# Kernel optimization log

Measured on AMD Instinct MI355X. Metric: run time of the kernel, lower is better.

## Reference

```python
import jax, jax.numpy as jnp
import numpy as np

N_NODES = 50000
N_EDGES = 800000
OBS_DIM = 25
HID = 128
EMB = 64
EDGE_DIM = 8
HEADS = 4
N_LAYERS = 3
COMM_RANGE = 1500.0
LN_EPS = 1e-5


def layernorm(x, g, b):
    mu = jnp.mean(x, axis=-1, keepdims=True)
    var = jnp.mean((x - mu) ** 2, axis=-1, keepdims=True)
    return (x - mu) / jnp.sqrt(var + LN_EPS) * g + b


def setup_inputs() -> dict:
    key = jax.random.key(0)
    ks = iter(jax.random.split(key, 64))

    def w(shape, s=0.05):
        return (jax.random.normal(next(ks), shape, jnp.float32) * s).astype(jnp.float32)

    inp = {}
    inp["observations"] = jax.random.normal(next(ks), (N_NODES, OBS_DIM), jnp.float32)
    inp["positions"] = jax.random.uniform(next(ks), (N_NODES, 2), jnp.float32) * 1000.0
    inp["edge_index"] = jax.random.randint(next(ks), (2, N_EDGES), 0, N_NODES, jnp.int32)
    # node encoder (obs_encoder branch: Linear-LN-ReLU-Linear-ReLU)
    inp["enc_w1"] = w((OBS_DIM, HID)); inp["enc_b1"] = w((HID,), 0.01)
    inp["enc_ln_g"] = jnp.ones((HID,), jnp.float32); inp["enc_ln_b"] = jnp.zeros((HID,), jnp.float32)
    inp["enc_w2"] = w((HID, EMB)); inp["enc_b2"] = w((EMB,), 0.01)
    cat_dim = 2 * EMB + EDGE_DIM  # 136
    # per-layer GNN params, stacked over layers
    inp["msg_w1"] = w((N_LAYERS, cat_dim, HID)); inp["msg_b1"] = w((N_LAYERS, HID), 0.01)
    inp["msg_w2"] = w((N_LAYERS, HID, EMB)); inp["msg_b2"] = w((N_LAYERS, EMB), 0.01)
    inp["att_w1"] = w((N_LAYERS, cat_dim, HID)); inp["att_b1"] = w((N_LAYERS, HID), 0.01)
    inp["att_w2"] = w((N_LAYERS, HID, HEADS)); inp["att_b2"] = w((N_LAYERS, HEADS), 0.01)
    inp["upd_w1"] = w((N_LAYERS, 2 * EMB, HID)); inp["upd_b1"] = w((N_LAYERS, HID), 0.01)
    inp["upd_w2"] = w((N_LAYERS, HID, EMB)); inp["upd_b2"] = w((N_LAYERS, EMB), 0.01)
    inp["ln_g"] = jnp.ones((N_LAYERS, EMB), jnp.float32); inp["ln_b"] = jnp.zeros((N_LAYERS, EMB), jnp.float32)
    # output projection
    inp["out_w1"] = w((EMB, HID)); inp["out_b1"] = w((HID,), 0.01)
    inp["out_w2"] = w((HID, EMB)); inp["out_b2"] = w((EMB,), 0.01)
    return inp


def reference(observations, positions, edge_index,
              enc_w1, enc_b1, enc_ln_g, enc_ln_b, enc_w2, enc_b2,
              msg_w1, msg_b1, msg_w2, msg_b2,
              att_w1, att_b1, att_w2, att_b2,
              upd_w1, upd_b1, upd_w2, upd_b2,
              ln_g, ln_b,
              out_w1, out_b1, out_w2, out_b2):
    n = observations.shape[0]
    # --- node encoder (use_full_obs=True path) ---
    h = observations @ enc_w1 + enc_b1
    h = jax.nn.relu(layernorm(h, enc_ln_g, enc_ln_b))
    x = jax.nn.relu(h @ enc_w2 + enc_b2)  # [N, EMB]

    # --- edge features (build_graph math, edges given) ---
    src, dst = edge_index[0], edge_index[1]
    rel = positions[dst] - positions[src]                    # [E, 2]
    dist = jnp.linalg.norm(rel, axis=-1, keepdims=True)      # [E, 1]
    rel_n = rel / (dist + 1e-6)
    dist_n = dist / COMM_RANGE
    angle = jnp.arctan2(rel[:, 1], rel[:, 0])[:, None]
    edge_attr = jnp.concatenate(
        [dist_n, rel_n, jnp.cos(angle), jnp.sin(angle), dist_n ** 2,
         jnp.zeros((rel.shape[0], 2), x.dtype)], axis=-1)    # [E, 8]

    # --- GNN communication layers (PyG: x_i = target = dst, x_j = source = src,
    #     aggregate to dst; dropout inactive at inference) ---
    for l in range(N_LAYERS):
        cat = jnp.concatenate([x[dst], x[src], edge_attr], axis=-1)       # [E, 136]
        m = jax.nn.relu(cat @ msg_w1[l] + msg_b1[l]) @ msg_w2[l] + msg_b2[l]   # [E, EMB]
        a = jax.nn.relu(cat @ att_w1[l] + att_b1[l]) @ att_w2[l] + att_b2[l]   # [E, HEADS]
        wgt = jnp.mean(jax.nn.softmax(a, axis=-1), axis=-1, keepdims=True)     # [E, 1]
        aggr = jax.ops.segment_sum(m * wgt, dst, num_segments=n)               # [N, EMB]
        upd_in = jnp.concatenate([x, aggr], axis=-1)                            # [N, 2*EMB]
        upd = jax.nn.relu(upd_in @ upd_w1[l] + upd_b1[l]) @ upd_w2[l] + upd_b2[l]
        x = layernorm(x + upd, ln_g[l], ln_b[l])

    # --- output projection ---
    return jax.nn.relu(x @ out_w1 + out_b1) @ out_w2 + out_b2
```

## Files before the change

kernel.cpp:

```cpp
#include <hip/hip_runtime.h>
#include <hip/hip_bf16.h>

typedef unsigned short ushort_t;
typedef unsigned int uint_t;

constexpr int OBS  = 25;
constexpr int HID  = 128;
constexpr int EMB  = 64;
constexpr int CAT  = 136;
constexpr int NN   = 50000;
constexpr int HALF = NN / 2;
constexpr int NK   = 2 * NN;

constexpr int TE      = 128;
constexpr int ETHR    = 256;
constexpr int K1PAD   = 148;
constexpr int K2PAD   = 140;
constexpr int K1STEPS = 9;
constexpr int K2STEPS = 8;

constexpr int TB = 128;

typedef __attribute__((ext_vector_type(8)))  short bf16x8;
typedef __attribute__((ext_vector_type(16))) float f32x16;
typedef __attribute__((ext_vector_type(4)))  uint_t uint4v;
typedef __attribute__((ext_vector_type(4)))  float f32x4;

__device__ __forceinline__ ushort_t f2bf(float f) {
    union { float f; uint_t u; } v; v.f = f;
    uint_t r = v.u + 0x7FFFu + ((v.u >> 16) & 1u);
    return (ushort_t)(r >> 16);
}

__device__ __forceinline__ bf16x8 ld8(const ushort_t* p) {
    uint2 lo = *reinterpret_cast<const uint2*>(p);
    uint2 hi = *reinterpret_cast<const uint2*>(p + 4);
    uint4 u = make_uint4(lo.x, lo.y, hi.x, hi.y);
    return __builtin_bit_cast(bf16x8, u);
}

#define CROW(R, LHI) (4 * (LHI) + ((R) & 3) + 8 * ((R) >> 2))

__global__ __launch_bounds__(256) void k_hist(
    const int* __restrict__ src, const int* __restrict__ dst,
    int* __restrict__ hist, int ne)
{
    int e = blockIdx.x * 256 + threadIdx.x;
    if (e < ne) {
        int key = (src[e] >= HALF ? NN : 0) + dst[e];
        atomicAdd(&hist[key], 1);
    }
}

__global__ __launch_bounds__(512) void k_scan1(
    const int* __restrict__ hist, int* __restrict__ scanned,
    int* __restrict__ bsum, int nk)
{
    __shared__ int s[512];
    int t = threadIdx.x, i = blockIdx.x * 512 + t;
    int v = (i < nk) ? hist[i] : 0;
    s[t] = v; __syncthreads();
#pragma unroll
    for (int off = 1; off < 512; off <<= 1) {
        int x = (t >= off) ? s[t - off] : 0;
        __syncthreads();
        s[t] += x;
        __syncthreads();
    }
    if (i < nk) scanned[i] = s[t] - v;
    if (t == 511) bsum[blockIdx.x] = s[511];
}

__global__ __launch_bounds__(512) void k_scan3(
    int* __restrict__ scanned, const int* __restrict__ bsum, int nk)
{
    __shared__ int pref;
    if (threadIdx.x == 0) {
        int run = 0;
        for (int b = 0; b < blockIdx.x; ++b) run += bsum[b];
        pref = run;
    }
    __syncthreads();
    int i = blockIdx.x * 512 + threadIdx.x;
    if (i < nk) scanned[i] += pref;
}

__global__ __launch_bounds__(256) void k_scatter_feat(
    const float* __restrict__ pos, const int* __restrict__ src,
    const int* __restrict__ dst, int* __restrict__ ofs,
    uint4v* __restrict__ eab4, int ne)
{
    int e = blockIdx.x * 256 + threadIdx.x;
    if (e >= ne) return;
    int s = src[e], d = dst[e];
    float rx = pos[d * 2 + 0] - pos[s * 2 + 0];
    float ry = pos[d * 2 + 1] - pos[s * 2 + 1];
    float dist = sqrtf(rx * rx + ry * ry);
    float inv = 1.f / (dist + 1e-6f);
    float dn = dist * (1.f / 1500.f);
    uint_t ux = (uint_t)f2bf(dn) | ((uint_t)f2bf(rx * inv) << 16);
    uint_t uy = (uint_t)f2bf(ry * inv) | ((dist > 0.f ? 0u : 1u) << 16);
    int key = (s >= HALF ? NN : 0) + d;
    int p = atomicAdd(&ofs[key], 1);
    uint4v ev = { ux, uy, (uint_t)s, (uint_t)d };
    __builtin_nontemporal_store(ev, eab4 + p);
}

__global__ __launch_bounds__(256) void k_prep(
    const float* __restrict__ w1, const float* __restrict__ w2,
    ushort_t* __restrict__ w1t, ushort_t* __restrict__ w2t)
{
    int t = blockIdx.x * 256 + threadIdx.x;
    const int n1 = 3 * HID * K1PAD;
    if (t < n1) {
        int l = t / (HID * K1PAD), rem = t % (HID * K1PAD);
        int c = rem / K1PAD, k = rem % K1PAD;
        float v = (k < CAT) ? w1[(size_t)l * CAT * HID + (size_t)k * HID + c] : 0.f;
        w1t[t] = f2bf(v);
    }
    const int n2 = 3 * EMB * K2PAD;
    if (t < n2) {
        int l = t / (EMB * K2PAD), rem = t % (EMB * K2PAD);
        int c = rem / K2PAD, k = rem % K2PAD;
        float v = (k < HID) ? w2[(size_t)l * HID * EMB + (size_t)k * EMB + c] : 0.f;
        w2t[t] = f2bf(v);
    }
}

constexpr int EKP = 36;
__global__ __launch_bounds__(256, 1) void k_encoder_mfma(
    const float* __restrict__ obs,
    const float* __restrict__ w1, const float* __restrict__ b1,
    const float* __restrict__ lng, const float* __restrict__ lnb,
    const float* __restrict__ w2, const float* __restrict__ b2,
    float* __restrict__ x, ushort_t* __restrict__ xb, int n)
{
    __shared__ __align__(16) ushort_t s_OB[TB * EKP];
    __shared__ __align__(16) ushort_t s_B1[HID * EKP];
    __shared__ __align__(16) float    s_G[TB * 132];
    __shared__ __align__(16) ushort_t s_H[TB * K2PAD];
    __shared__ __align__(16) ushort_t s_W2[EMB * K2PAD];

    const int tid = threadIdx.x;
    const int lane = tid & 63, wid = tid >> 6;
    const int wr = wid >> 1, wc = wid & 1;
    const int l31 = lane & 31, lhi = lane >> 5;
    const int n0 = blockIdx.x * TB;

    for (int i = tid; i < TB * 32; i += 256) {
        int row = i >> 5, k = i & 31;
        int gn = n0 + row;
        float v = (gn < n && k < OBS) ? obs[(size_t)gn * OBS + k] : 0.f;
        s_OB[row * EKP + k] = f2bf(v);
    }
    for (int i = tid; i < 32 * HID; i += 256) {
        int k = i >> 7, c = i & 127;
        float v = (k < OBS) ? w1[k * HID + c] : 0.f;
        s_B1[c * EKP + k] = f2bf(v);
    }
    __syncthreads();

    f32x16 a00, a01, a10, a11;
    {
        float bv0 = b1[wc * 64 + l31], bv1 = b1[wc * 64 + 32 + l31];
#pragma unroll
        for (int i = 0; i < 16; ++i) { a00[i] = bv0; a01[i] = bv1; a10[i] = bv0; a11[i] = bv1; }
    }
    {
        const ushort_t* aR0 = s_OB + (wr * 64 + l31) * EKP;
        const ushort_t* aR1 = aR0 + 32 * EKP;
        const ushort_t* bR0 = s_B1 + (wc * 64 + l31) * EKP;
        const ushort_t* bR1 = bR0 + 32 * EKP;
        const int koff = lhi * 8;
#pragma unroll
        for (int s = 0; s < 2; ++s) {
            const int ke = s * 16 + koff;
            bf16x8 av0 = ld8(aR0 + ke), av1 = ld8(aR1 + ke);
            bf16x8 bv0 = ld8(bR0 + ke), bv1 = ld8(bR1 + ke);
            a00 = __builtin_amdgcn_mfma_f32_32x32x16_bf16(av0, bv0, a00, 0, 0, 0);
            a01 = __builtin_amdgcn_mfma_f32_32x32x16_bf16(av0, bv1, a01, 0, 0, 0);
            a10 = __builtin_amdgcn_mfma_f32_32x32x16_bf16(av1, bv0, a10, 0, 0, 0);
            a11 = __builtin_amdgcn_mfma_f32_32x32x16_bf16(av1, bv1, a11, 0, 0, 0);
        }
    }
#define WRITE_G(ACC, SUB, NC)                                                  \
    {                                                                          \
        const int col = wc * 64 + (NC) * 32 + l31;                             \
        _Pragma("unroll")                                                      \
        for (int r = 0; r < 16; ++r) {                                         \
            int row = wr * 64 + (SUB) * 32 + CROW(r, lhi);                     \
            s_G[row * 132 + col] = ACC[r];                                     \
        }                                                                      \
    }
    WRITE_G(a00, 0, 0) WRITE_G(a01, 0, 1) WRITE_G(a10, 1, 0) WRITE_G(a11, 1, 1)
#undef WRITE_G
    __syncthreads();

    for (int i = tid; i < HID * EMB; i += 256) {
        int k = i >> 6, c = i & 63;
        s_W2[c * K2PAD + k] = f2bf(w2[i]);
    }
    if (tid < TB) {
        float sum = 0.f, sum2 = 0.f;
        const float* gr = s_G + tid * 132;
#pragma unroll 8
        for (int q = 0; q < HID; ++q) { float v = gr[q]; sum += v; sum2 += v * v; }
        float mu = sum * (1.f / HID);
        float var = fmaxf(sum2 * (1.f / HID) - mu * mu, 0.f);
        float rs = 1.f / sqrtf(var + 1e-5f);
        ushort_t* hr = s_H + tid * K2PAD;
#pragma unroll 8
        for (int q = 0; q < HID; ++q) {
            float v = (gr[q] - mu) * rs * lng[q] + lnb[q];
            hr[q] = f2bf(fmaxf(v, 0.f));
        }
    }
    __syncthreads();

    f32x16 c0, c1;
    {
        float bv = b2[wc * 32 + l31];
#pragma unroll
        for (int i = 0; i < 16; ++i) { c0[i] = bv; c1[i] = bv; }
    }
    {
        const ushort_t* aR0 = s_H + (wr * 64 + l31) * K2PAD;
        const ushort_t* aR1 = aR0 + 32 * K2PAD;
        const ushort_t* bR = s_W2 + (wc * 32 + l31) * K2PAD;
        const int koff = lhi * 8;
#pragma unroll
        for (int s = 0; s < K2STEPS; ++s) {
            const int ke = s * 16 + koff;
            bf16x8 av0 = ld8(aR0 + ke), av1 = ld8(aR1 + ke);
            bf16x8 bv = ld8(bR + ke);
            c0 = __builtin_amdgcn_mfma_f32_32x32x16_bf16(av0, bv, c0, 0, 0, 0);
            c1 = __builtin_amdgcn_mfma_f32_32x32x16_bf16(av1, bv, c1, 0, 0, 0);
        }
    }
    {
        const int col = wc * 32 + l31;
#define STORE_X(CC, SUB)                                                       \
        {                                                                      \
            _Pragma("unroll")                                                  \
            for (int r = 0; r < 16; ++r) {                                     \
                int row = wr * 64 + (SUB) * 32 + CROW(r, lhi);                 \
                int gn = n0 + row;                                             \
                if (gn < n) {                                                  \
                    float v = fmaxf(CC[r], 0.f);                               \
                    x[(size_t)gn * EMB + col] = v;                             \
                    xb[(size_t)gn * EMB + col] = f2bf(v);                      \
                }                                                              \
            }                                                                  \
        }
        STORE_X(c0, 0) STORE_X(c1, 1)
#undef STORE_X
    }
}

__global__ __launch_bounds__(ETHR, 4) void k_edge_mfma(
    const ushort_t* __restrict__ xb,
    const uint4v* __restrict__ eab4,
    const ushort_t* __restrict__ w1t,
    const float* __restrict__ b1,
    const ushort_t* __restrict__ w2t,
    const float* __restrict__ b2,
    float* __restrict__ aggr, int ne)
{
    __shared__ __align__(16) ushort_t s_A[TE * K1PAD];
    __shared__ int s_dst[TE];
    ushort_t* s_H = s_A;
    float*    s_M = reinterpret_cast<float*>(s_A);

    const int tid  = threadIdx.x;
    const int lane = tid & 63, wid = tid >> 6;
    const int wr = wid >> 1, wc = wid & 1;
    const int l31 = lane & 31, lhi = lane >> 5;

    const int nwg = ne / TE;
    const int q = nwg >> 3, rr = nwg & 7;
    const int bid = blockIdx.x;
    const int xcd = bid & 7, loc = bid >> 3;
    const int swz = (xcd < rr ? xcd * (q + 1) : rr * (q + 1) + (xcd - rr) * q) + loc;
    const int e0 = swz * TE;

    {
        const int e = tid >> 1, h = tid & 1, ge = e0 + e;
        ushort_t* arow = s_A + e * K1PAD;
        uint4v ev = __builtin_nontemporal_load(eab4 + ge);
        if (h == 0) {
            s_dst[e] = (int)ev.w;
            const uint2* sp = reinterpret_cast<const uint2*>(xb + (size_t)ev.w * EMB);
            uint2* dp = reinterpret_cast<uint2*>(arow);
#pragma unroll
            for (int i = 0; i < 16; ++i) dp[i] = sp[i];
        } else {
            const uint2* sp = reinterpret_cast<const uint2*>(xb + (size_t)ev.z * EMB);
            uint2* dp = reinterpret_cast<uint2*>(arow + EMB);
#pragma unroll
            for (int i = 0; i < 16; ++i) dp[i] = sp[i];
            uint_t dn_b = ev.x & 0xFFFFu, rxn_b = ev.x >> 16;
            uint_t ryn_b = ev.y & 0xFFFFu, flag = ev.y >> 16;
            uint_t cos_b = flag ? 0x3F80u : rxn_b;
            uint_t sin_b = flag ? 0u : ryn_b;
            union { uint_t u; float f; } cv; cv.u = dn_b << 16;
            uint_t dn2_b = (uint_t)f2bf(cv.f * cv.f);
            uint2* ap = reinterpret_cast<uint2*>(arow + 2 * EMB);
            ap[0] = make_uint2(dn_b | (rxn_b << 16), ryn_b | (cos_b << 16));
            ap[1] = make_uint2(sin_b | (dn2_b << 16), 0u);
            uint2* pp = reinterpret_cast<uint2*>(arow + CAT);
            pp[0] = make_uint2(0u, 0u); pp[1] = make_uint2(0u, 0u);
            pp[2] = make_uint2(0u, 0u);
        }
    }
    __syncthreads();

    f32x16 a00, a01, a10, a11;
    {
        float bv0 = b1[wc * 64 + l31], bv1 = b1[wc * 64 + 32 + l31];
#pragma unroll
        for (int i = 0; i < 16; ++i) { a00[i] = bv0; a01[i] = bv1; a10[i] = bv0; a11[i] = bv1; }
    }
    {
        const ushort_t* aR0 = s_A + (wr * 64 + l31) * K1PAD;
        const ushort_t* aR1 = aR0 + 32 * K1PAD;
        const ushort_t* bR0 = w1t + (wc * 64 + l31) * K1PAD;
        const ushort_t* bR1 = bR0 + 32 * K1PAD;
        const int koff = lhi * 8;
#pragma unroll
        for (int s = 0; s < K1STEPS; ++s) {
            const int ke = s * 16 + koff;
            bf16x8 av0 = ld8(aR0 + ke);
            bf16x8 av1 = ld8(aR1 + ke);
            bf16x8 bv0 = ld8(bR0 + ke);
            bf16x8 bv1 = ld8(bR1 + ke);
            a00 = __builtin_amdgcn_mfma_f32_32x32x16_bf16(av0, bv0, a00, 0, 0, 0);
            a01 = __builtin_amdgcn_mfma_f32_32x32x16_bf16(av0, bv1, a01, 0, 0, 0);
            a10 = __builtin_amdgcn_mfma_f32_32x32x16_bf16(av1, bv0, a10, 0, 0, 0);
            a11 = __builtin_amdgcn_mfma_f32_32x32x16_bf16(av1, bv1, a11, 0, 0, 0);
        }
    }
    __syncthreads();

#define WRITE_H(ACC, SUB, NC)                                                  \
    {                                                                          \
        const int col = wc * 64 + (NC) * 32 + l31;                             \
        _Pragma("unroll")                                                      \
        for (int r = 0; r < 16; ++r) {                                         \
            int row = wr * 64 + (SUB) * 32 + CROW(r, lhi);                     \
            s_H[row * K2PAD + col] = f2bf(fmaxf(ACC[r], 0.f));                 \
        }                                                                      \
    }
    WRITE_H(a00, 0, 0) WRITE_H(a01, 0, 1) WRITE_H(a10, 1, 0) WRITE_H(a11, 1, 1)
#undef WRITE_H
    __syncthreads();

    f32x16 c0, c1;
    {
        float bv = b2[wc * 32 + l31];
#pragma unroll
        for (int i = 0; i < 16; ++i) { c0[i] = bv; c1[i] = bv; }
    }
    {
        const ushort_t* aR0 = s_H + (wr * 64 + l31) * K2PAD;
        const ushort_t* aR1 = aR0 + 32 * K2PAD;
        const ushort_t* bR = w2t + (wc * 32 + l31) * K2PAD;
        const int koff = lhi * 8;
#pragma unroll
        for (int s = 0; s < K2STEPS; ++s) {
            const int ke = s * 16 + koff;
            bf16x8 av0 = ld8(aR0 + ke);
            bf16x8 av1 = ld8(aR1 + ke);
            bf16x8 bv = ld8(bR + ke);
            c0 = __builtin_amdgcn_mfma_f32_32x32x16_bf16(av0, bv, c0, 0, 0, 0);
            c1 = __builtin_amdgcn_mfma_f32_32x32x16_bf16(av1, bv, c1, 0, 0, 0);
        }
    }
    __syncthreads();

    {
        const int col = wc * 32 + l31;
#pragma unroll
        for (int r = 0; r < 16; ++r) {
            int row = wr * 64 + CROW(r, lhi);
            s_M[row * 68 + col] = c0[r] * 0.25f;
            s_M[(row + 32) * 68 + col] = c1[r] * 0.25f;
        }
    }
    __syncthreads();

    {
        const int col = tid & 63, g = tid >> 6, base = g * 32;
        int cur = s_dst[base];
        float acc = 0.f;
#pragma unroll 8
        for (int r = 0; r < 32; ++r) {
            int d = s_dst[base + r];
            float v = s_M[(base + r) * 68 + col];
            if (d != cur) {
                atomicAdd(aggr + (size_t)cur * EMB + col, acc);
                acc = 0.f; cur = d;
            }
            acc += v;
        }
        atomicAdd(aggr + (size_t)cur * EMB + col, acc);
    }
}

__global__ __launch_bounds__(256, 2) void k_update_mfma(
    float* __restrict__ x, ushort_t* __restrict__ xb,
    const float* __restrict__ aggr,
    const float* __restrict__ w1, const float* __restrict__ b1,
    const float* __restrict__ w2, const float* __restrict__ b2,
    const float* __restrict__ g, const float* __restrict__ bb, int n)
{
    __shared__ __align__(16) ushort_t s_A[TB * K2PAD];
    __shared__ __align__(16) ushort_t s_B[TB * K2PAD];
    ushort_t* s_H  = s_A;
    ushort_t* s_W2 = s_B;
    float*    s_U  = reinterpret_cast<float*>(s_B);

    const int tid = threadIdx.x;
    const int lane = tid & 63, wid = tid >> 6;
    const int wr = wid >> 1, wc = wid & 1;
    const int l31 = lane & 31, lhi = lane >> 5;
    const int n0 = blockIdx.x * TB;

    {
        const int row = tid >> 1, h = tid & 1;
        const int gn = n0 + row;
        ushort_t* arow = s_A + row * K2PAD;
        if (h == 0) {
            uint2* dp = reinterpret_cast<uint2*>(arow);
            if (gn < n) {
                const uint2* sp = reinterpret_cast<const uint2*>(xb + (size_t)gn * EMB);
#pragma unroll
                for (int i = 0; i < 16; ++i) dp[i] = sp[i];
            } else {
                const uint2 z = make_uint2(0u, 0u);
#pragma unroll
                for (int i = 0; i < 16; ++i) dp[i] = z;
            }
        } else {
            if (gn < n) {
                const f32x4* sp = reinterpret_cast<const f32x4*>(aggr + (size_t)gn * EMB);
#pragma unroll
                for (int i = 0; i < 16; ++i) {
                    f32x4 v = __builtin_nontemporal_load(sp + i);
                    ushort_t* qq = arow + EMB + i * 4;
                    qq[0] = f2bf(v.x); qq[1] = f2bf(v.y); qq[2] = f2bf(v.z); qq[3] = f2bf(v.w);
                }
            } else {
#pragma unroll
                for (int i = 0; i < 16; ++i) {
                    ushort_t* qq = arow + EMB + i * 4;
                    qq[0] = 0; qq[1] = 0; qq[2] = 0; qq[3] = 0;
                }
            }
        }
    }
    for (int i = tid; i < 128 * 128; i += 256) {
        int k = i >> 7, c = i & 127;
        s_B[c * K2PAD + k] = f2bf(w1[i]);
    }
    __syncthreads();

    f32x16 a00, a01, a10, a11;
    {
        float bv0 = b1[wc * 64 + l31], bv1 = b1[wc * 64 + 32 + l31];
#pragma unroll
        for (int i = 0; i < 16; ++i) { a00[i] = bv0; a01[i] = bv1; a10[i] = bv0; a11[i] = bv1; }
    }
    {
        const ushort_t* aR0 = s_A + (wr * 64 + l31) * K2PAD;
        const ushort_t* aR1 = aR0 + 32 * K2PAD;
        const ushort_t* bR0 = s_B + (wc * 64 + l31) * K2PAD;
        const ushort_t* bR1 = bR0 + 32 * K2PAD;
        const int koff = lhi * 8;
#pragma unroll
        for (int s = 0; s < K2STEPS; ++s) {
            const int ke = s * 16 + koff;
            bf16x8 av0 = ld8(aR0 + ke), av1 = ld8(aR1 + ke);
            bf16x8 bv0 = ld8(bR0 + ke), bv1 = ld8(bR1 + ke);
            a00 = __builtin_amdgcn_mfma_f32_32x32x16_bf16(av0, bv0, a00, 0, 0, 0);
            a01 = __builtin_amdgcn_mfma_f32_32x32x16_bf16(av0, bv1, a01, 0, 0, 0);
            a10 = __builtin_amdgcn_mfma_f32_32x32x16_bf16(av1, bv0, a10, 0, 0, 0);
            a11 = __builtin_amdgcn_mfma_f32_32x32x16_bf16(av1, bv1, a11, 0, 0, 0);
        }
    }
    __syncthreads();

#define WRITE_H(ACC, SUB, NC)                                                  \
    {                                                                          \
        const int col = wc * 64 + (NC) * 32 + l31;                             \
        _Pragma("unroll")                                                      \
        for (int r = 0; r < 16; ++r) {                                         \
            int row = wr * 64 + (SUB) * 32 + CROW(r, lhi);                     \
            s_H[row * K2PAD + col] = f2bf(fmaxf(ACC[r], 0.f));                 \
        }                                                                      \
    }
    WRITE_H(a00, 0, 0) WRITE_H(a01, 0, 1) WRITE_H(a10, 1, 0) WRITE_H(a11, 1, 1)
#undef WRITE_H
    for (int i = tid; i < HID * EMB; i += 256) {
        int k = i >> 6, c = i & 63;
        s_W2[c * K2PAD + k] = f2bf(w2[i]);
    }
    __syncthreads();

    f32x16 c0, c1;
    {
        float bv = b2[wc * 32 + l31];
#pragma unroll
        for (int i = 0; i < 16; ++i) { c0[i] = bv; c1[i] = bv; }
    }
    {
        const ushort_t* aR0 = s_H + (wr * 64 + l31) * K2PAD;
        const ushort_t* aR1 = aR0 + 32 * K2PAD;
        const ushort_t* bR = s_W2 + (wc * 32 + l31) * K2PAD;
        const int koff = lhi * 8;
#pragma unroll
        for (int s = 0; s < K2STEPS; ++s) {
            const int ke = s * 16 + koff;
            bf16x8 av0 = ld8(aR0 + ke), av1 = ld8(aR1 + ke);
            bf16x8 bv = ld8(bR + ke);
            c0 = __builtin_amdgcn_mfma_f32_32x32x16_bf16(av0, bv, c0, 0, 0, 0);
            c1 = __builtin_amdgcn_mfma_f32_32x32x16_bf16(av1, bv, c1, 0, 0, 0);
        }
    }
    __syncthreads();

    {
        const int col = wc * 32 + l31;
#pragma unroll
        for (int r = 0; r < 16; ++r) {
            int row = wr * 64 + CROW(r, lhi);
            s_U[row * 68 + col] = c0[r];
            s_U[(row + 32) * 68 + col] = c1[r];
        }
    }
    __syncthreads();

    if (tid < TB) {
        int gn = n0 + tid;
        if (gn < n) {
            const float* xr = x + (size_t)gn * EMB;
            float* ur = s_U + tid * 68;
            float sum = 0.f, sum2 = 0.f;
#pragma unroll 8
            for (int q = 0; q < EMB; ++q) {
                float v = xr[q] + ur[q];
                ur[q] = v;
                sum += v; sum2 += v * v;
            }
            float mu = sum * (1.f / EMB);
            float var = fmaxf(sum2 * (1.f / EMB) - mu * mu, 0.f);
            float rs = 1.f / sqrtf(var + 1e-5f);
            float* xo = x + (size_t)gn * EMB;
            ushort_t* xbo = xb + (size_t)gn * EMB;
#pragma unroll 8
            for (int q = 0; q < EMB; ++q) {
                float v = (ur[q] - mu) * rs * g[q] + bb[q];
                xo[q] = v;
                xbo[q] = f2bf(v);
            }
        }
    }
}

constexpr int OKP = 68;
__global__ __launch_bounds__(256, 2) void k_output_mfma(
    const ushort_t* __restrict__ xb,
    const float* __restrict__ w1, const float* __restrict__ b1,
    const float* __restrict__ w2, const float* __restrict__ b2,
    float* __restrict__ out, int n)
{
    __shared__ __align__(16) ushort_t s_A[TB * OKP];
    __shared__ __align__(16) ushort_t s_B[HID * OKP];
    __shared__ __align__(16) ushort_t s_H[TB * K2PAD];
    __shared__ __align__(16) ushort_t s_W2[EMB * K2PAD];

    const int tid = threadIdx.x;
    const int lane = tid & 63, wid = tid >> 6;
    const int wr = wid >> 1, wc = wid & 1;
    const int l31 = lane & 31, lhi = lane >> 5;
    const int n0 = blockIdx.x * TB;

    for (int i = tid; i < TB * 16; i += 256) {
        int row = i >> 4, q = i & 15;
        int gn = n0 + row;
        uint2 v = make_uint2(0u, 0u);
        if (gn < n) v = reinterpret_cast<const uint2*>(xb + (size_t)gn * EMB)[q];
        *reinterpret_cast<uint2*>(s_A + row * OKP + q * 4) = v;
    }
    for (int i = tid; i < EMB * HID; i += 256) {
        int k = i >> 7, c = i & 127;
        s_B[c * OKP + k] = f2bf(w1[i]);
    }
    for (int i = tid; i < HID * EMB; i += 256) {
        int k = i >> 6, c = i & 63;
        s_W2[c * K2PAD + k] = f2bf(w2[i]);
    }
    __syncthreads();

    f32x16 a00, a01, a10, a11;
    {
        float bv0 = b1[wc * 64 + l31], bv1 = b1[wc * 64 + 32 + l31];
#pragma unroll
        for (int i = 0; i < 16; ++i) { a00[i] = bv0; a01[i] = bv1; a10[i] = bv0; a11[i] = bv1; }
    }
    {
        const ushort_t* aR0 = s_A + (wr * 64 + l31) * OKP;
        const ushort_t* aR1 = aR0 + 32 * OKP;
        const ushort_t* bR0 = s_B + (wc * 64 + l31) * OKP;
        const ushort_t* bR1 = bR0 + 32 * OKP;
        const int koff = lhi * 8;
#pragma unroll
        for (int s = 0; s < 4; ++s) {
            const int ke = s * 16 + koff;
            bf16x8 av0 = ld8(aR0 + ke), av1 = ld8(aR1 + ke);
            bf16x8 bv0 = ld8(bR0 + ke), bv1 = ld8(bR1 + ke);
            a00 = __builtin_amdgcn_mfma_f32_32x32x16_bf16(av0, bv0, a00, 0, 0, 0);
            a01 = __builtin_amdgcn_mfma_f32_32x32x16_bf16(av0, bv1, a01, 0, 0, 0);
            a10 = __builtin_amdgcn_mfma_f32_32x32x16_bf16(av1, bv0, a10, 0, 0, 0);
            a11 = __builtin_amdgcn_mfma_f32_32x32x16_bf16(av1, bv1, a11, 0, 0, 0);
        }
    }
    __syncthreads();

#define WRITE_H(ACC, SUB, NC)                                                  \
    {                                                                          \
        const int col = wc * 64 + (NC) * 32 + l31;                             \
        _Pragma("unroll")                                                      \
        for (int r = 0; r < 16; ++r) {                                         \
            int row = wr * 64 + (SUB) * 32 + CROW(r, lhi);                     \
            s_H[row * K2PAD + col] = f2bf(fmaxf(ACC[r], 0.f));                 \
        }                                                                      \
    }
    WRITE_H(a00, 0, 0) WRITE_H(a01, 0, 1) WRITE_H(a10, 1, 0) WRITE_H(a11, 1, 1)
#undef WRITE_H
    __syncthreads();

    f32x16 c0, c1;
    {
        float bv = b2[wc * 32 + l31];
#pragma unroll
        for (int i = 0; i < 16; ++i) { c0[i] = bv; c1[i] = bv; }
    }
    {
        const ushort_t* aR0 = s_H + (wr * 64 + l31) * K2PAD;
        const ushort_t* aR1 = aR0 + 32 * K2PAD;
        const ushort_t* bR = s_W2 + (wc * 32 + l31) * K2PAD;
        const int koff = lhi * 8;
#pragma unroll
        for (int s = 0; s < K2STEPS; ++s) {
            const int ke = s * 16 + koff;
            bf16x8 av0 = ld8(aR0 + ke), av1 = ld8(aR1 + ke);
            bf16x8 bv = ld8(bR + ke);
            c0 = __builtin_amdgcn_mfma_f32_32x32x16_bf16(av0, bv, c0, 0, 0, 0);
            c1 = __builtin_amdgcn_mfma_f32_32x32x16_bf16(av1, bv, c1, 0, 0, 0);
        }
    }
    {
        const int col = wc * 32 + l31;
#pragma unroll
        for (int r = 0; r < 16; ++r) {
            int row0 = wr * 64 + CROW(r, lhi);
            int g0 = n0 + row0, g1 = g0 + 32;
            if (g0 < n) out[(size_t)g0 * EMB + col] = c0[r];
            if (g1 < n) out[(size_t)g1 * EMB + col] = c1[r];
        }
    }
}

extern "C" void kernel_launch(void* const* d_in, const int* in_sizes, int n_in,
                              void* d_out, int out_size, void* d_ws, size_t ws_size,
                              hipStream_t stream)
{
    const float* obs     = (const float*)d_in[0];
    const float* pos     = (const float*)d_in[1];
    const int*   eidx    = (const int*)d_in[2];
    const float* enc_w1  = (const float*)d_in[3];
    const float* enc_b1  = (const float*)d_in[4];
    const float* enc_lng = (const float*)d_in[5];
    const float* enc_lnb = (const float*)d_in[6];
    const float* enc_w2  = (const float*)d_in[7];
    const float* enc_b2  = (const float*)d_in[8];
    const float* msg_w1  = (const float*)d_in[9];
    const float* msg_b1  = (const float*)d_in[10];
    const float* msg_w2  = (const float*)d_in[11];
    const float* msg_b2  = (const float*)d_in[12];
    const float* upd_w1  = (const float*)d_in[17];
    const float* upd_b1  = (const float*)d_in[18];
    const float* upd_w2  = (const float*)d_in[19];
    const float* upd_b2  = (const float*)d_in[20];
    const float* ln_g    = (const float*)d_in[21];
    const float* ln_b    = (const float*)d_in[22];
    const float* out_w1  = (const float*)d_in[23];
    const float* out_b1  = (const float*)d_in[24];
    const float* out_w2  = (const float*)d_in[25];
    const float* out_b2  = (const float*)d_in[26];

    const int n  = in_sizes[0] / OBS;
    const int ne = in_sizes[2] / 2;
    const int* src = eidx;
    const int* dst = eidx + ne;

    char* ws = (char*)d_ws;
    float*    x     = (float*)ws;
    ushort_t* xbuf  = (ushort_t*)(ws + 12800000);
    uint4v*   eab4  = (uint4v*)(ws + 19200000);
    float*    aggr  = (float*)(ws + 32000000);
    ushort_t* w1t   = (ushort_t*)(ws + 44800000);
    ushort_t* w2t   = (ushort_t*)(ws + 44913664);
    int*      hist  = (int*)(ws + 44967424);
    int*      scan  = (int*)(ws + 45367424);
    int*      bsum  = (int*)(ws + 45767424);

    const int NB1 = (NK + 511) / 512;
    const int nb  = (n + TB - 1) / TB;

    hipMemsetAsync(hist, 0, NK * sizeof(int), stream);
    k_hist<<<(ne + 255) / 256, 256, 0, stream>>>(src, dst, hist, ne);
    k_scan1<<<NB1, 512, 0, stream>>>(hist, scan, bsum, NK);
    k_scan3<<<NB1, 512, 0, stream>>>(scan, bsum, NK);
    k_scatter_feat<<<(ne + 255) / 256, 256, 0, stream>>>(pos, src, dst, scan,
                                                         eab4, ne);

    k_prep<<<(3 * HID * K1PAD + 255) / 256, 256, 0, stream>>>(msg_w1, msg_w2, w1t, w2t);
    k_encoder_mfma<<<nb, 256, 0, stream>>>(obs, enc_w1, enc_b1, enc_lng, enc_lnb,
                                           enc_w2, enc_b2, x, xbuf, n);

    for (int l = 0; l < 3; ++l) {
        hipMemsetAsync(aggr, 0, (size_t)n * EMB * sizeof(float), stream);
        k_edge_mfma<<<ne / TE, ETHR, 0, stream>>>(
            xbuf, eab4,
            w1t + (size_t)l * HID * K1PAD, msg_b1 + (size_t)l * HID,
            w2t + (size_t)l * EMB * K2PAD, msg_b2 + (size_t)l * EMB,
            aggr, ne);
        k_update_mfma<<<nb, 256, 0, stream>>>(
            x, xbuf, aggr,
            upd_w1 + (size_t)l * 2 * EMB * HID, upd_b1 + (size_t)l * HID,
            upd_w2 + (size_t)l * HID * EMB, upd_b2 + (size_t)l * EMB,
            ln_g + (size_t)l * EMB, ln_b + (size_t)l * EMB, n);
    }
    k_output_mfma<<<nb, 256, 0, stream>>>(
        xbuf, out_w1, out_b1, out_w2, out_b2, (float*)d_out, n);
}
```

Measured before the change: 795.3 us.

## Partition edge kernel by destination-node CSR ranges with LDS accumulation

Builds a CSR row pointer over destination nodes and gives each edge block a fixed range of 7 nodes, looping over that range's edges in 128-edge tiles. Results are reduced in shared memory and written straight to aggr. This removes the per-layer memset and the global float atomics. In exchange, tiles are padded with zeroed rows whenever a node range's edge count is not a multiple of the tile, which wastes MFMA work. The earlier sort by source-half, which helped gather locality, is also dropped.

```diff
diff --git a/kernel.cpp b/kernel.cpp
--- a/kernel.cpp
+++ b/kernel.cpp
@@ -3,14 +3,14 @@
 
 typedef unsigned short ushort_t;
 typedef unsigned int uint_t;
+typedef unsigned char uchar_t;
 
 constexpr int OBS  = 25;
 constexpr int HID  = 128;
 constexpr int EMB  = 64;
 constexpr int CAT  = 136;
 constexpr int NN   = 50000;
-constexpr int HALF = NN / 2;
-constexpr int NK   = 2 * NN;
+constexpr int NPB  = 7;
 
 constexpr int TE      = 128;
 constexpr int ETHR    = 256;
@@ -42,14 +42,10 @@
 #define CROW(R, LHI) (4 * (LHI) + ((R) & 3) + 8 * ((R) >> 2))
 
 __global__ __launch_bounds__(256) void k_hist(
-    const int* __restrict__ src, const int* __restrict__ dst,
-    int* __restrict__ hist, int ne)
+    const int* __restrict__ dst, int* __restrict__ hist, int ne)
 {
     int e = blockIdx.x * 256 + threadIdx.x;
-    if (e < ne) {
-        int key = (src[e] >= HALF ? NN : 0) + dst[e];
-        atomicAdd(&hist[key], 1);
-    }
+    if (e < ne) atomicAdd(&hist[dst[e]], 1);
 }
 
 __global__ __launch_bounds__(512) void k_scan1(
@@ -72,17 +68,23 @@
 }
 
 __global__ __launch_bounds__(512) void k_scan3(
-    int* __restrict__ scanned, const int* __restrict__ bsum, int nk)
+    int* __restrict__ scanned, const int* __restrict__ bsum,
+    int* __restrict__ rowptr, int nk, int ne)
 {
     __shared__ int pref;
     if (threadIdx.x == 0) {
         int run = 0;
-        for (int b = 0; b < blockIdx.x; ++b) run += bsum[b];
+        for (int b = 0; b < (int)blockIdx.x; ++b) run += bsum[b];
         pref = run;
     }
     __syncthreads();
     int i = blockIdx.x * 512 + threadIdx.x;
-    if (i < nk) scanned[i] += pref;
+    if (i < nk) {
+        int v = scanned[i] + pref;
+        scanned[i] = v;
+        rowptr[i] = v;
+    }
+    if (blockIdx.x == 0 && threadIdx.x == 0) rowptr[nk] = ne;
 }
 
 __global__ __launch_bounds__(256) void k_scatter_feat(
@@ -100,8 +102,7 @@
     float dn = dist * (1.f / 1500.f);
     uint_t ux = (uint_t)f2bf(dn) | ((uint_t)f2bf(rx * inv) << 16);
     uint_t uy = (uint_t)f2bf(ry * inv) | ((dist > 0.f ? 0u : 1u) << 16);
-    int key = (s >= HALF ? NN : 0) + d;
-    int p = atomicAdd(&ofs[key], 1);
+    int p = atomicAdd(&ofs[d], 1);
     uint4v ev = { ux, uy, (uint_t)s, (uint_t)d };
     __builtin_nontemporal_store(ev, eab4 + p);
 }
@@ -260,14 +261,16 @@
 __global__ __launch_bounds__(ETHR, 4) void k_edge_mfma(
     const ushort_t* __restrict__ xb,
     const uint4v* __restrict__ eab4,
+    const int* __restrict__ rowptr,
     const ushort_t* __restrict__ w1t,
     const float* __restrict__ b1,
     const ushort_t* __restrict__ w2t,
     const float* __restrict__ b2,
-    float* __restrict__ aggr, int ne)
+    float* __restrict__ aggr, int nwg)
 {
     __shared__ __align__(16) ushort_t s_A[TE * K1PAD];
-    __shared__ int s_dst[TE];
+    __shared__ float   s_acc[8 * 64];
+    __shared__ uchar_t s_ld[TE];
     ushort_t* s_H = s_A;
     float*    s_M = reinterpret_cast<float*>(s_A);
 
@@ -276,133 +279,165 @@
     const int wr = wid >> 1, wc = wid & 1;
     const int l31 = lane & 31, lhi = lane >> 5;
 
-    const int nwg = ne / TE;
     const int q = nwg >> 3, rr = nwg & 7;
     const int bid = blockIdx.x;
     const int xcd = bid & 7, loc = bid >> 3;
     const int swz = (xcd < rr ? xcd * (q + 1) : rr * (q + 1) + (xcd - rr) * q) + loc;
-    const int e0 = swz * TE;
-
-    {
-        const int e = tid >> 1, h = tid & 1, ge = e0 + e;
-        ushort_t* arow = s_A + e * K1PAD;
-        uint4v ev = __builtin_nontemporal_load(eab4 + ge);
-        if (h == 0) {
-            s_dst[e] = (int)ev.w;
-            const uint2* sp = reinterpret_cast<const uint2*>(xb + (size_t)ev.w * EMB);
-            uint2* dp = reinterpret_cast<uint2*>(arow);
-#pragma unroll
-            for (int i = 0; i < 16; ++i) dp[i] = sp[i];
-        } else {
-            const uint2* sp = reinterpret_cast<const uint2*>(xb + (size_t)ev.z * EMB);
-            uint2* dp = reinterpret_cast<uint2*>(arow + EMB);
-#pragma unroll
-            for (int i = 0; i < 16; ++i) dp[i] = sp[i];
-            uint_t dn_b = ev.x & 0xFFFFu, rxn_b = ev.x >> 16;
-            uint_t ryn_b = ev.y & 0xFFFFu, flag = ev.y >> 16;
-            uint_t cos_b = flag ? 0x3F80u : rxn_b;
-            uint_t sin_b = flag ? 0u : ryn_b;
-            union { uint_t u; float f; } cv; cv.u = dn_b << 16;
-            uint_t dn2_b = (uint_t)f2bf(cv.f * cv.f);
-            uint2* ap = reinterpret_cast<uint2*>(arow + 2 * EMB);
-            ap[0] = make_uint2(dn_b | (rxn_b << 16), ryn_b | (cos_b << 16));
-            ap[1] = make_uint2(sin_b | (dn2_b << 16), 0u);
-            uint2* pp = reinterpret_cast<uint2*>(arow + CAT);
-            pp[0] = make_uint2(0u, 0u); pp[1] = make_uint2(0u, 0u);
-            pp[2] = make_uint2(0u, 0u);
-        }
-    }
-    __syncthreads();
-
-    f32x16 a00, a01, a10, a11;
-    {
-        float bv0 = b1[wc * 64 + l31], bv1 = b1[wc * 64 + 32 + l31];
-#pragma unroll
-        for (int i = 0; i < 16; ++i) { a00[i] = bv0; a01[i] = bv1; a10[i] = bv0; a11[i] = bv1; }
-    }
-    {
-        const ushort_t* aR0 = s_A + (wr * 64 + l31) * K1PAD;
-        const ushort_t* aR1 = aR0 + 32 * K1PAD;
-        const ushort_t* bR0 = w1t + (wc * 64 + l31) * K1PAD;
-        const ushort_t* bR1 = bR0 + 32 * K1PAD;
-        const int koff = lhi * 8;
-#pragma unroll
-        for (int s = 0; s < K1STEPS; ++s) {
-            const int ke = s * 16 + koff;
-            bf16x8 av0 = ld8(aR0 + ke);
-            bf16x8 av1 = ld8(aR1 + ke);
-            bf16x8 bv0 = ld8(bR0 + ke);
-            bf16x8 bv1 = ld8(bR1 + ke);
-            a00 = __builtin_amdgcn_mfma_f32_32x32x16_bf16(av0, bv0, a00, 0, 0, 0);
-            a01 = __builtin_amdgcn_mfma_f32_32x32x16_bf16(av0, bv1, a01, 0, 0, 0);
-            a10 = __builtin_amdgcn_mfma_f32_32x32x16_bf16(av1, bv0, a10, 0, 0, 0);
-            a11 = __builtin_amdgcn_mfma_f32_32x32x16_bf16(av1, bv1, a11, 0, 0, 0);
-        }
-    }
-    __syncthreads();
+
+    const int n0 = swz * NPB;
+    const int n1 = min(n0 + NPB, NN);
+    const int eb0 = rowptr[n0];
+    const int ee  = rowptr[n1];
+
+    for (int i = tid; i < 8 * 64; i += ETHR) s_acc[i] = 0.f;
+
+    for (int eb = eb0; eb < ee; eb += TE) {
+        {
+            const int e = tid >> 1, h = tid & 1, ge = eb + e;
+            ushort_t* arow = s_A + e * K1PAD;
+            if (ge < ee) {
+                uint4v ev = eab4[ge];
+                if (h == 0) {
+                    s_ld[e] = (uchar_t)((int)ev.w - n0);
+                    const uint2* sp = reinterpret_cast<const uint2*>(xb + (size_t)ev.w * EMB);
+                    uint2* dp = reinterpret_cast<uint2*>(arow);
+#pragma unroll
+                    for (int i = 0; i < 16; ++i) dp[i] = sp[i];
+                } else {
+                    const uint2* sp = reinterpret_cast<const uint2*>(xb + (size_t)ev.z * EMB);
+                    uint2* dp = reinterpret_cast<uint2*>(arow + EMB);
+#pragma unroll
+                    for (int i = 0; i < 16; ++i) dp[i] = sp[i];
+                    uint_t dn_b = ev.x & 0xFFFFu, rxn_b = ev.x >> 16;
+                    uint_t ryn_b = ev.y & 0xFFFFu, flag = ev.y >> 16;
+                    uint_t cos_b = flag ? 0x3F80u : rxn_b;
+                    uint_t sin_b = flag ? 0u : ryn_b;
+                    union { uint_t u; float f; } cv; cv.u = dn_b << 16;
+                    uint_t dn2_b = (uint_t)f2bf(cv.f * cv.f);
+                    uint2* ap = reinterpret_cast<uint2*>(arow + 2 * EMB);
+                    ap[0] = make_uint2(dn_b | (rxn_b << 16), ryn_b | (cos_b << 16));
+                    ap[1] = make_uint2(sin_b | (dn2_b << 16), 0u);
+                    uint2* pp = reinterpret_cast<uint2*>(arow + CAT);
+                    pp[0] = make_uint2(0u, 0u); pp[1] = make_uint2(0u, 0u);
+                    pp[2] = make_uint2(0u, 0u);
+                }
+            } else {
+                const uint2 z = make_uint2(0u, 0u);
+                if (h == 0) {
+                    s_ld[e] = 7;
+                    uint2* dp = reinterpret_cast<uint2*>(arow);
+#pragma unroll
+                    for (int i = 0; i < 16; ++i) dp[i] = z;
+                } else {
+                    uint2* dp = reinterpret_cast<uint2*>(arow + EMB);
+#pragma unroll
+                    for (int i = 0; i < 16; ++i) dp[i] = z;
+                    uint2* ap = reinterpret_cast<uint2*>(arow + 2 * EMB);
+                    ap[0] = z; ap[1] = z;
+                    uint2* pp = reinterpret_cast<uint2*>(arow + CAT);
+                    pp[0] = z; pp[1] = z; pp[2] = z;
+                }
+            }
+        }
+        __syncthreads();
+
+        f32x16 a00, a01, a10, a11;
+        {
+            float bv0 = b1[wc * 64 + l31], bv1 = b1[wc * 64 + 32 + l31];
+#pragma unroll
+            for (int i = 0; i < 16; ++i) { a00[i] = bv0; a01[i] = bv1; a10[i] = bv0; a11[i] = bv1; }
+        }
+        {
+            const ushort_t* aR0 = s_A + (wr * 64 + l31) * K1PAD;
+            const ushort_t* aR1 = aR0 + 32 * K1PAD;
+            const ushort_t* bR0 = w1t + (wc * 64 + l31) * K1PAD;
+            const ushort_t* bR1 = bR0 + 32 * K1PAD;
+            const int koff = lhi * 8;
+#pragma unroll
+            for (int s = 0; s < K1STEPS; ++s) {
+                const int ke = s * 16 + koff;
+                bf16x8 av0 = ld8(aR0 + ke);
+                bf16x8 av1 = ld8(aR1 + ke);
+                bf16x8 bv0 = ld8(bR0 + ke);
+                bf16x8 bv1 = ld8(bR1 + ke);
+                a00 = __builtin_amdgcn_mfma_f32_32x32x16_bf16(av0, bv0, a00, 0, 0, 0);
+                a01 = __builtin_amdgcn_mfma_f32_32x32x16_bf16(av0, bv1, a01, 0, 0, 0);
+                a10 = __builtin_amdgcn_mfma_f32_32x32x16_bf16(av1, bv0, a10, 0, 0, 0);
+                a11 = __builtin_amdgcn_mfma_f32_32x32x16_bf16(av1, bv1, a11, 0, 0, 0);
+            }
+        }
+        __syncthreads();
 
 #define WRITE_H(ACC, SUB, NC)                                                  \
-    {                                                                          \
-        const int col = wc * 64 + (NC) * 32 + l31;                             \
-        _Pragma("unroll")                                                      \
-        for (int r = 0; r < 16; ++r) {                                         \
-            int row = wr * 64 + (SUB) * 32 + CROW(r, lhi);                     \
-            s_H[row * K2PAD + col] = f2bf(fmaxf(ACC[r], 0.f));                 \
-        }                                                                      \
-    }
-    WRITE_H(a00, 0, 0) WRITE_H(a01, 0, 1) WRITE_H(a10, 1, 0) WRITE_H(a11, 1, 1)
+        {                                                                      \
+            const int col = wc * 64 + (NC) * 32 + l31;                         \
+            _Pragma("unroll")                                                  \
+            for (int r = 0; r < 16; ++r) {                                     \
+                int row = wr * 64 + (SUB) * 32 + CROW(r, lhi);                 \
+                s_H[row * K2PAD + col] = f2bf(fmaxf(ACC[r], 0.f));             \
+            }                                                                  \
+        }
+        WRITE_H(a00, 0, 0) WRITE_H(a01, 0, 1) WRITE_H(a10, 1, 0) WRITE_H(a11, 1, 1)
 #undef WRITE_H
-    __syncthreads();
-
-    f32x16 c0, c1;
-    {
-        float bv = b2[wc * 32 + l31];
-#pragma unroll
-        for (int i = 0; i < 16; ++i) { c0[i] = bv; c1[i] = bv; }
-    }
-    {
-        const ushort_t* aR0 = s_H + (wr * 64 + l31) * K2PAD;
-        const ushort_t* aR1 = aR0 + 32 * K2PAD;
-        const ushort_t* bR = w2t + (wc * 32 + l31) * K2PAD;
-        const int koff = lhi * 8;
-#pragma unroll
-        for (int s = 0; s < K2STEPS; ++s) {
-            const int ke = s * 16 + koff;
-            bf16x8 av0 = ld8(aR0 + ke);
-            bf16x8 av1 = ld8(aR1 + ke);
-            bf16x8 bv = ld8(bR + ke);
-            c0 = __builtin_amdgcn_mfma_f32_32x32x16_bf16(av0, bv, c0, 0, 0, 0);
-            c1 = __builtin_amdgcn_mfma_f32_32x32x16_bf16(av1, bv, c1, 0, 0, 0);
-        }
-    }
-    __syncthreads();
-
-    {
-        const int col = wc * 32 + l31;
-#pragma unroll
-        for (int r = 0; r < 16; ++r) {
-            int row = wr * 64 + CROW(r, lhi);
-            s_M[row * 68 + col] = c0[r] * 0.25f;
-            s_M[(row + 32) * 68 + col] = c1[r] * 0.25f;
-        }
-    }
-    __syncthreads();
-
-    {
-        const int col = tid & 63, g = tid >> 6, base = g * 32;
-        int cur = s_dst[base];
-        float acc = 0.f;
+        __syncthreads();
+
+        f32x16 c0, c1;
+        {
+            float bv = b2[wc * 32 + l31];
+#pragma unroll
+            for (int i = 0; i < 16; ++i) { c0[i] = bv; c1[i] = bv; }
+        }
+        {
+            const ushort_t* aR0 = s_H + (wr * 64 + l31) * K2PAD;
+            const ushort_t* aR1 = aR0 + 32 * K2PAD;
+            const ushort_t* bR = w2t + (wc * 32 + l31) * K2PAD;
+            const int koff = lhi * 8;
+#pragma unroll
+            for (int s = 0; s < K2STEPS; ++s) {
+                const int ke = s * 16 + koff;
+                bf16x8 av0 = ld8(aR0 + ke);
+                bf16x8 av1 = ld8(aR1 + ke);
+                bf16x8 bv = ld8(bR + ke);
+                c0 = __builtin_amdgcn_mfma_f32_32x32x16_bf16(av0, bv, c0, 0, 0, 0);
+                c1 = __builtin_amdgcn_mfma_f32_32x32x16_bf16(av1, bv, c1, 0, 0, 0);
+            }
+        }
+        __syncthreads();
+
+        {
+            const int col = wc * 32 + l31;
+#pragma unroll
+            for (int r = 0; r < 16; ++r) {
+                int row = wr * 64 + CROW(r, lhi);
+                s_M[row * 68 + col] = c0[r] * 0.25f;
+                s_M[(row + 32) * 68 + col] = c1[r] * 0.25f;
+            }
+        }
+        __syncthreads();
+
+        {
+            const int col = tid & 63, g = tid >> 6, base = g * 32;
+            int cur = s_ld[base];
+            float accv = 0.f;
 #pragma unroll 8
-        for (int r = 0; r < 32; ++r) {
-            int d = s_dst[base + r];
-            float v = s_M[(base + r) * 68 + col];
-            if (d != cur) {
-                atomicAdd(aggr + (size_t)cur * EMB + col, acc);
-                acc = 0.f; cur = d;
-            }
-            acc += v;
-        }
-        atomicAdd(aggr + (size_t)cur * EMB + col, acc);
+            for (int r = 0; r < 32; ++r) {
+                int d = s_ld[base + r];
+                float v = s_M[(base + r) * 68 + col];
+                if (d != cur) {
+                    atomicAdd(&s_acc[cur * 64 + col], accv);
+                    accv = 0.f; cur = d;
+                }
+                accv += v;
+            }
+            atomicAdd(&s_acc[cur * 64 + col], accv);
+        }
+        __syncthreads();
+    }
+
+    for (int i = tid; i < NPB * 64; i += ETHR) {
+        int r = i >> 6, c = i & 63;
+        int gn = n0 + r;
+        if (gn < NN) aggr[(size_t)gn * EMB + c] = s_acc[r * 64 + c];
     }
 }
 
@@ -705,23 +740,25 @@
     const int* dst = eidx + ne;
 
     char* ws = (char*)d_ws;
-    float*    x     = (float*)ws;
-    ushort_t* xbuf  = (ushort_t*)(ws + 12800000);
-    uint4v*   eab4  = (uint4v*)(ws + 19200000);
-    float*    aggr  = (float*)(ws + 32000000);
-    ushort_t* w1t   = (ushort_t*)(ws + 44800000);
-    ushort_t* w2t   = (ushort_t*)(ws + 44913664);
-    int*      hist  = (int*)(ws + 44967424);
-    int*      scan  = (int*)(ws + 45367424);
-    int*      bsum  = (int*)(ws + 45767424);
-
-    const int NB1 = (NK + 511) / 512;
+    float*    x      = (float*)ws;
+    ushort_t* xbuf   = (ushort_t*)(ws + 12800000);
+    uint4v*   eab4   = (uint4v*)(ws + 19200000);
+    float*    aggr   = (float*)(ws + 32000000);
+    ushort_t* w1t    = (ushort_t*)(ws + 44800000);
+    ushort_t* w2t    = (ushort_t*)(ws + 44913664);
+    int*      hist   = (int*)(ws + 44967424);
+    int*      scan   = (int*)(ws + 45167424);
+    int*      rowptr = (int*)(ws + 45367424);
+    int*      bsum   = (int*)(ws + 45567432);
+
+    const int NB1 = (NN + 511) / 512;
     const int nb  = (n + TB - 1) / TB;
-
-    hipMemsetAsync(hist, 0, NK * sizeof(int), stream);
-    k_hist<<<(ne + 255) / 256, 256, 0, stream>>>(src, dst, hist, ne);
-    k_scan1<<<NB1, 512, 0, stream>>>(hist, scan, bsum, NK);
-    k_scan3<<<NB1, 512, 0, stream>>>(scan, bsum, NK);
+    const int nbe = (NN + NPB - 1) / NPB;
+
+    hipMemsetAsync(hist, 0, NN * sizeof(int), stream);
+    k_hist<<<(ne + 255) / 256, 256, 0, stream>>>(dst, hist, ne);
+    k_scan1<<<NB1, 512, 0, stream>>>(hist, scan, bsum, NN);
+    k_scan3<<<NB1, 512, 0, stream>>>(scan, bsum, rowptr, NN, ne);
     k_scatter_feat<<<(ne + 255) / 256, 256, 0, stream>>>(pos, src, dst, scan,
                                                          eab4, ne);
 
@@ -730,12 +767,11 @@
                                            enc_w2, enc_b2, x, xbuf, n);
 
     for (int l = 0; l < 3; ++l) {
-        hipMemsetAsync(aggr, 0, (size_t)n * EMB * sizeof(float), stream);
-        k_edge_mfma<<<ne / TE, ETHR, 0, stream>>>(
-            xbuf, eab4,
+        k_edge_mfma<<<nbe, ETHR, 0, stream>>>(
+            xbuf, eab4, rowptr,
             w1t + (size_t)l * HID * K1PAD, msg_b1 + (size_t)l * HID,
             w2t + (size_t)l * EMB * K2PAD, msg_b2 + (size_t)l * EMB,
-            aggr, ne);
+            aggr, nbe);
         k_update_mfma<<<nb, 256, 0, stream>>>(
             x, xbuf, aggr,
             upd_w1 + (size_t)l * 2 * EMB * HID, upd_b1 + (size_t)l * HID,
```

After: 1.759 ms. 2.21x slower.

## Simplify edge sort to dst-only keys and zero aggr inside update kernel

Applied to the files above, without the earlier changes.

Edge ordering now uses only the destination node as the counting-sort key, dropping the split by source half. That removes a larger histogram and scan and drops the src read in k_hist. The edge kernel goes back to plain block indexing without XCD swizzling, and nontemporal loads and stores are replaced by normal ones. The per-layer memset of aggr is replaced by having the update kernel zero aggr after reading it, which saves a full pass over that buffer each layer. The risks are worse source-side locality in x gathers and different L2 behaviour across XCDs.

```diff
diff --git a/kernel.cpp b/kernel.cpp
--- a/kernel.cpp
+++ b/kernel.cpp
@@ -9,8 +9,6 @@
 constexpr int EMB  = 64;
 constexpr int CAT  = 136;
 constexpr int NN   = 50000;
-constexpr int HALF = NN / 2;
-constexpr int NK   = 2 * NN;
 
 constexpr int TE      = 128;
 constexpr int ETHR    = 256;
@@ -24,7 +22,6 @@
 typedef __attribute__((ext_vector_type(8)))  short bf16x8;
 typedef __attribute__((ext_vector_type(16))) float f32x16;
 typedef __attribute__((ext_vector_type(4)))  uint_t uint4v;
-typedef __attribute__((ext_vector_type(4)))  float f32x4;
 
 __device__ __forceinline__ ushort_t f2bf(float f) {
     union { float f; uint_t u; } v; v.f = f;
@@ -42,14 +39,10 @@
 #define CROW(R, LHI) (4 * (LHI) + ((R) & 3) + 8 * ((R) >> 2))
 
 __global__ __launch_bounds__(256) void k_hist(
-    const int* __restrict__ src, const int* __restrict__ dst,
-    int* __restrict__ hist, int ne)
+    const int* __restrict__ dst, int* __restrict__ hist, int ne)
 {
     int e = blockIdx.x * 256 + threadIdx.x;
-    if (e < ne) {
-        int key = (src[e] >= HALF ? NN : 0) + dst[e];
-        atomicAdd(&hist[key], 1);
-    }
+    if (e < ne) atomicAdd(&hist[dst[e]], 1);
 }
 
 __global__ __launch_bounds__(512) void k_scan1(
@@ -77,7 +70,7 @@
     __shared__ int pref;
     if (threadIdx.x == 0) {
         int run = 0;
-        for (int b = 0; b < blockIdx.x; ++b) run += bsum[b];
+        for (int b = 0; b < (int)blockIdx.x; ++b) run += bsum[b];
         pref = run;
     }
     __syncthreads();
@@ -100,10 +93,9 @@
     float dn = dist * (1.f / 1500.f);
     uint_t ux = (uint_t)f2bf(dn) | ((uint_t)f2bf(rx * inv) << 16);
     uint_t uy = (uint_t)f2bf(ry * inv) | ((dist > 0.f ? 0u : 1u) << 16);
-    int key = (s >= HALF ? NN : 0) + d;
-    int p = atomicAdd(&ofs[key], 1);
+    int p = atomicAdd(&ofs[d], 1);
     uint4v ev = { ux, uy, (uint_t)s, (uint_t)d };
-    __builtin_nontemporal_store(ev, eab4 + p);
+    eab4[p] = ev;
 }
 
 __global__ __launch_bounds__(256) void k_prep(
@@ -275,18 +267,12 @@
     const int lane = tid & 63, wid = tid >> 6;
     const int wr = wid >> 1, wc = wid & 1;
     const int l31 = lane & 31, lhi = lane >> 5;
-
-    const int nwg = ne / TE;
-    const int q = nwg >> 3, rr = nwg & 7;
-    const int bid = blockIdx.x;
-    const int xcd = bid & 7, loc = bid >> 3;
-    const int swz = (xcd < rr ? xcd * (q + 1) : rr * (q + 1) + (xcd - rr) * q) + loc;
-    const int e0 = swz * TE;
+    const int e0 = blockIdx.x * TE;
 
     {
         const int e = tid >> 1, h = tid & 1, ge = e0 + e;
         ushort_t* arow = s_A + e * K1PAD;
-        uint4v ev = __builtin_nontemporal_load(eab4 + ge);
+        uint4v ev = eab4[ge];
         if (h == 0) {
             s_dst[e] = (int)ev.w;
             const uint2* sp = reinterpret_cast<const uint2*>(xb + (size_t)ev.w * EMB);
@@ -408,7 +394,7 @@
 
 __global__ __launch_bounds__(256, 2) void k_update_mfma(
     float* __restrict__ x, ushort_t* __restrict__ xb,
-    const float* __restrict__ aggr,
+    float* __restrict__ aggr,
     const float* __restrict__ w1, const float* __restrict__ b1,
     const float* __restrict__ w2, const float* __restrict__ b2,
     const float* __restrict__ g, const float* __restrict__ bb, int n)
@@ -442,10 +428,12 @@
             }
         } else {
             if (gn < n) {
-                const f32x4* sp = reinterpret_cast<const f32x4*>(aggr + (size_t)gn * EMB);
+                float4* sp = reinterpret_cast<float4*>(aggr + (size_t)gn * EMB);
+                const float4 z4 = make_float4(0.f, 0.f, 0.f, 0.f);
 #pragma unroll
                 for (int i = 0; i < 16; ++i) {
-                    f32x4 v = __builtin_nontemporal_load(sp + i);
+                    float4 v = sp[i];
+                    sp[i] = z4;
                     ushort_t* qq = arow + EMB + i * 4;
                     qq[0] = f2bf(v.x); qq[1] = f2bf(v.y); qq[2] = f2bf(v.z); qq[3] = f2bf(v.w);
                 }
@@ -712,25 +700,25 @@
     ushort_t* w1t   = (ushort_t*)(ws + 44800000);
     ushort_t* w2t   = (ushort_t*)(ws + 44913664);
     int*      hist  = (int*)(ws + 44967424);
-    int*      scan  = (int*)(ws + 45367424);
-    int*      bsum  = (int*)(ws + 45767424);
-
-    const int NB1 = (NK + 511) / 512;
+    int*      scan  = (int*)(ws + 45167424);
+    int*      bsum  = (int*)(ws + 45367424);
+
+    const int NB1 = (NN + 511) / 512;
     const int nb  = (n + TB - 1) / TB;
 
-    hipMemsetAsync(hist, 0, NK * sizeof(int), stream);
-    k_hist<<<(ne + 255) / 256, 256, 0, stream>>>(src, dst, hist, ne);
-    k_scan1<<<NB1, 512, 0, stream>>>(hist, scan, bsum, NK);
-    k_scan3<<<NB1, 512, 0, stream>>>(scan, bsum, NK);
+    hipMemsetAsync(hist, 0, NN * sizeof(int), stream);
+    k_hist<<<(ne + 255) / 256, 256, 0, stream>>>(dst, hist, ne);
+    k_scan1<<<NB1, 512, 0, stream>>>(hist, scan, bsum, NN);
+    k_scan3<<<NB1, 512, 0, stream>>>(scan, bsum, NN);
     k_scatter_feat<<<(ne + 255) / 256, 256, 0, stream>>>(pos, src, dst, scan,
                                                          eab4, ne);
 
     k_prep<<<(3 * HID * K1PAD + 255) / 256, 256, 0, stream>>>(msg_w1, msg_w2, w1t, w2t);
     k_encoder_mfma<<<nb, 256, 0, stream>>>(obs, enc_w1, enc_b1, enc_lng, enc_lnb,
                                            enc_w2, enc_b2, x, xbuf, n);
+    hipMemsetAsync(aggr, 0, (size_t)n * EMB * sizeof(float), stream);
 
     for (int l = 0; l < 3; ++l) {
-        hipMemsetAsync(aggr, 0, (size_t)n * EMB * sizeof(float), stream);
         k_edge_mfma<<<ne / TE, ETHR, 0, stream>>>(
             xbuf, eab4,
             w1t + (size_t)l * HID * K1PAD, msg_b1 + (size_t)l * HID,
```

Result: faster. 754.9 us (-5.1%).
